# Performance work log

Measured on AMD Instinct MI355X. Metric: run time of the kernel, lower is better.

## Reference

```python
import jax, jax.numpy as jnp
import numpy as np

N, F = 16384, 32
H1, H2, D1, D2 = 64, 64, 32, 1


def setup_inputs() -> dict:
    key = jax.random.key(0)
    ks = jax.random.split(key, 10)
    x = jax.random.normal(ks[0], (N, F), dtype=jnp.float32)
    # pre-normalized adjacency (GCNConv expects D^-1/2 A D^-1/2); mimic with uniform/N
    a = jax.random.uniform(ks[1], (N, N), dtype=jnp.float32) / N
    # glorot-ish scaled params
    W1 = jax.random.normal(ks[2], (F, H1), dtype=jnp.float32) * (1.0 / np.sqrt(F))
    b1 = jnp.zeros((H1,), dtype=jnp.float32)
    W2 = jax.random.normal(ks[3], (H1, H2), dtype=jnp.float32) * (1.0 / np.sqrt(H1))
    b2 = jnp.zeros((H2,), dtype=jnp.float32)
    Wd1 = jax.random.normal(ks[4], (H2, D1), dtype=jnp.float32) * (1.0 / np.sqrt(H2))
    bd1 = jnp.zeros((D1,), dtype=jnp.float32)
    Wd2 = jax.random.normal(ks[5], (D1, D2), dtype=jnp.float32) * (1.0 / np.sqrt(D1))
    bd2 = jnp.zeros((D2,), dtype=jnp.float32)
    return {"x": x, "a": a, "W1": W1, "b1": b1, "W2": W2, "b2": b2,
            "Wd1": Wd1, "bd1": bd1, "Wd2": Wd2, "bd2": bd2}


def reference(x, a, W1, b1, W2, b2, Wd1, bd1, Wd2, bd2):
    # GCNConv: relu(a @ (x @ W) + b)   (a is pre-normalized)
    g1 = jax.nn.relu(a @ (x @ W1) + b1)   # [N, 64]
    g2 = jax.nn.relu(a @ (g1 @ W2) + b2)  # [N, 64]
    d3 = jax.nn.relu(g2 @ Wd1 + bd1)      # [N, 32]
    return d3 @ Wd2 + bd2                 # [N, 1]
```

## Files before the change

kernel.cpp:

```cpp
#include <hip/hip_runtime.h>
#include <hip/hip_bf16.h>


typedef __bf16 bf16x8 __attribute__((ext_vector_type(8)));
typedef float  f32x16 __attribute__((ext_vector_type(16)));
typedef float  f32x4v __attribute__((ext_vector_type(4)));
typedef int    i32x4  __attribute__((ext_vector_type(4)));

#define NNODE 16384
#define KDIM  16384
#define HCOL  64

__device__ inline i32x4 pack8(f32x4v a, f32x4v b){
  bf16x8 t;
  t[0]=(__bf16)a[0]; t[1]=(__bf16)a[1]; t[2]=(__bf16)a[2]; t[3]=(__bf16)a[3];
  t[4]=(__bf16)b[0]; t[5]=(__bf16)b[1]; t[6]=(__bf16)b[2]; t[7]=(__bf16)b[3];
  return __builtin_bit_cast(i32x4, t);
}

__global__ __launch_bounds__(128) void gcn_layer_kernel(
    const float* __restrict__ A,
    const __bf16* __restrict__ Ht,
    const float* __restrict__ bias,
    float* __restrict__ G)
{
  __shared__ i32x4 sA[2*2*256];
  __shared__ i32x4 sH[2*2*512];

  const int tid  = threadIdx.x;
  const int lane = tid & 63;
  const int kw   = tid >> 6;
  const int row0 = blockIdx.x * 32;

  const int rA0  = lane >> 3;
  const int ccA  = lane & 7;
  const int swzA = ccA ^ rA0;
  const int r    = lane & 31;
  const int hsub = lane >> 5;
  const int xs   = lane & 7;

  const size_t k0base = (size_t)kw * 8192;

  f32x4v ra[8]; i32x4 rh[8];

  const float* pA0 = A + (size_t)(row0 + rA0) * KDIM + k0base + (size_t)ccA*8;
  const i32x4* pH0 = (const i32x4*)Ht + (size_t)rA0 * (KDIM/8) + k0base/8 + ccA;

  auto stage_load = [&](int t){
    const float* pA = pA0 + (size_t)t*64;
    #pragma unroll
    for (int pi=0; pi<4; ++pi){
      const float* p = pA + (size_t)pi*8*KDIM;
      ra[2*pi]   = __builtin_nontemporal_load((const f32x4v*)p);
      ra[2*pi+1] = __builtin_nontemporal_load((const f32x4v*)(p+4));
    }
    const i32x4* pH = pH0 + (size_t)t*8;
    #pragma unroll
    for (int pi=0; pi<8; ++pi)
      rh[pi] = pH[(size_t)pi*8*(KDIM/8)];
  };

  auto stage_write = [&](int buf){
    i32x4* dA = &sA[(kw*2+buf)*256];
    #pragma unroll
    for (int pi=0; pi<4; ++pi)
      dA[(rA0 + pi*8)*8 + swzA] = pack8(ra[2*pi], ra[2*pi+1]);
    i32x4* dH = &sH[(kw*2+buf)*512];
    #pragma unroll
    for (int pi=0; pi<8; ++pi)
      dH[(rA0 + pi*8)*8 + swzA] = rh[pi];
  };

  f32x16 acc0 = {}; f32x16 acc1 = {};

  auto compute = [&](int buf){
    const i32x4* bA = &sA[(kw*2+buf)*256];
    const i32x4* bH = &sH[(kw*2+buf)*512];
    #pragma unroll
    for (int kk=0; kk<4; ++kk){
      int c = (kk*2 + hsub) ^ xs;
      bf16x8 a  = __builtin_bit_cast(bf16x8, bA[r*8 + c]);
      bf16x8 b0 = __builtin_bit_cast(bf16x8, bH[r*8 + c]);
      bf16x8 b1 = __builtin_bit_cast(bf16x8, bH[(r+32)*8 + c]);
      acc0 = __builtin_amdgcn_mfma_f32_32x32x16_bf16(a, b0, acc0, 0,0,0);
      acc1 = __builtin_amdgcn_mfma_f32_32x32x16_bf16(a, b1, acc1, 0,0,0);
    }
  };

  stage_load(0);
  stage_write(0);
  __syncthreads();
  for (int t=0; t<127; ++t){
    stage_load(t+1);
    compute(t&1);
    __syncthreads();
    stage_write((t+1)&1);
    __syncthreads();
  }
  compute(1);
  __syncthreads();

  float* red = (float*)sA;
  if (kw == 1){
    #pragma unroll
    for (int j=0; j<16; ++j){
      int rr = (j&3) + 8*(j>>2) + 4*hsub;
      red[rr*64 + r]      = acc0[j];
      red[rr*64 + 32 + r] = acc1[j];
    }
  }
  __syncthreads();
  if (kw == 0){
    #pragma unroll
    for (int j=0; j<16; ++j){
      int rr = (j&3) + 8*(j>>2) + 4*hsub;
      float v0 = acc0[j] + red[rr*64 + r]      + bias[r];
      float v1 = acc1[j] + red[rr*64 + 32 + r] + bias[32 + r];
      G[(size_t)(row0 + rr)*HCOL + r]      = fmaxf(v0, 0.f);
      G[(size_t)(row0 + rr)*HCOL + 32 + r] = fmaxf(v1, 0.f);
    }
  }
}

template<int F>
__global__ __launch_bounds__(128) void proj_T_kernel(
    const float* __restrict__ in,
    const float* __restrict__ W,
    __bf16* __restrict__ out)
{
  constexpr int FP = F + 4;
  __shared__ float sWt[64*FP];
  __shared__ short sOut[64*136];

  int tid = threadIdx.x;
  for (int e = tid; e < 64*F; e += 128){
    int h = e / F, j = e - h*F;
    sWt[h*FP + j] = W[j*64 + h];
  }
  __syncthreads();

  const size_t n = (size_t)blockIdx.x*128 + tid;
  float rowv[F];
  #pragma unroll
  for (int j=0; j<F; j+=4){
    f32x4v v = *(const f32x4v*)(in + n*F + j);
    rowv[j]=v[0]; rowv[j+1]=v[1]; rowv[j+2]=v[2]; rowv[j+3]=v[3];
  }
  #pragma unroll
  for (int h=0; h<64; ++h){
    float s = 0.f;
    #pragma unroll
    for (int j=0; j<F; j+=4){
      f32x4v w = *(const f32x4v*)&sWt[h*FP + j];
      s += rowv[j]*w[0] + rowv[j+1]*w[1] + rowv[j+2]*w[2] + rowv[j+3]*w[3];
    }
    sOut[h*136 + tid] = __builtin_bit_cast(short, (__bf16)s);
  }
  __syncthreads();

  const size_t n0 = (size_t)blockIdx.x*128;
  #pragma unroll
  for (int pi=0; pi<8; ++pi){
    int p = pi*128 + tid;
    int h = p >> 4, cc = p & 15;
    i32x4 v = *(const i32x4*)&sOut[h*136 + cc*8];
    *(i32x4*)(out + (size_t)h*NNODE + n0 + cc*8) = v;
  }
}

__global__ __launch_bounds__(256) void tail_kernel(
    const float* __restrict__ g2,
    const float* __restrict__ Wd1,
    const float* __restrict__ bd1,
    const float* __restrict__ Wd2,
    const float* __restrict__ bd2,
    float* __restrict__ outp)
{
  __shared__ float sW[64*32];
  __shared__ float sb1[32], sw2[32];
  int tid = threadIdx.x;
  for (int e=tid; e<2048; e+=256) sW[e] = Wd1[e];
  if (tid < 32){ sb1[tid] = bd1[tid]; sw2[tid] = Wd2[tid]; }
  __syncthreads();

  size_t n = (size_t)blockIdx.x*256 + tid;
  float rv[64];
  #pragma unroll
  for (int j=0;j<64;j+=4){
    f32x4v v = *(const f32x4v*)(g2 + n*64 + j);
    rv[j]=v[0]; rv[j+1]=v[1]; rv[j+2]=v[2]; rv[j+3]=v[3];
  }
  float o = 0.f;
  #pragma unroll
  for (int c=0;c<32;++c){
    float s = sb1[c];
    #pragma unroll
    for (int j=0;j<64;++j) s += rv[j]*sW[j*32 + c];
    o += fmaxf(s, 0.f) * sw2[c];
  }
  outp[n] = o + bd2[0];
}

extern "C" void kernel_launch(void* const* d_in, const int* in_sizes, int n_in,
                              void* d_out, int out_size, void* d_ws, size_t ws_size,
                              hipStream_t stream)
{
  const float* x   = (const float*)d_in[0];
  const float* a   = (const float*)d_in[1];
  const float* W1  = (const float*)d_in[2];
  const float* b1  = (const float*)d_in[3];
  const float* W2  = (const float*)d_in[4];
  const float* b2  = (const float*)d_in[5];
  const float* Wd1 = (const float*)d_in[6];
  const float* bd1 = (const float*)d_in[7];
  const float* Wd2 = (const float*)d_in[8];
  const float* bd2 = (const float*)d_in[9];
  float* outp = (float*)d_out;

  char* ws = (char*)d_ws;
  __bf16* Ht1 = (__bf16*)(ws);
  __bf16* Ht2 = (__bf16*)(ws + (2u<<20));
  float*  g1  = (float*)(ws + (4u<<20));
  float*  g2  = (float*)(ws + (8u<<20));

  proj_T_kernel<32><<<128, 128, 0, stream>>>(x,  W1, Ht1);
  gcn_layer_kernel <<<512, 128, 0, stream>>>(a, Ht1, b1, g1);
  proj_T_kernel<64><<<128, 128, 0, stream>>>(g1, W2, Ht2);
  gcn_layer_kernel <<<512, 128, 0, stream>>>(a, Ht2, b2, g2);
  tail_kernel      <<<64, 256, 0, stream>>>(g2, Wd1, bd1, Wd2, bd2, outp);
}
```

Measured before the change: 505.9 us.

## Deepen register prefetch to two stages and halve barriers per k-step

Adds a second register buffer so global loads of A and Ht are issued two k-stages ahead of the MFMA compute. Shared-memory writes for the next buffer are interleaved with compute on the other buffer, which drops from two to one __syncthreads per stage. The aim is to hide more HBM latency in this bandwidth-bound aggregation and cut barrier stalls. In exchange it uses more VGPRs and issues a few redundant clamped loads at the tail.

```diff
diff --git a/kernel.cpp b/kernel.cpp
--- a/kernel.cpp
+++ b/kernel.cpp
@@ -41,26 +41,26 @@
 
   const size_t k0base = (size_t)kw * 8192;
 
-  f32x4v ra[8]; i32x4 rh[8];
+  f32x4v ra0[8], ra1[8]; i32x4 rh0[8], rh1[8];
 
   const float* pA0 = A + (size_t)(row0 + rA0) * KDIM + k0base + (size_t)ccA*8;
   const i32x4* pH0 = (const i32x4*)Ht + (size_t)rA0 * (KDIM/8) + k0base/8 + ccA;
 
-  auto stage_load = [&](int t){
-    const float* pA = pA0 + (size_t)t*64;
+  auto stage_load = [&](int idx, f32x4v (&ra)[8], i32x4 (&rh)[8]){
+    const float* pA = pA0 + (size_t)idx*64;
     #pragma unroll
     for (int pi=0; pi<4; ++pi){
       const float* p = pA + (size_t)pi*8*KDIM;
       ra[2*pi]   = __builtin_nontemporal_load((const f32x4v*)p);
       ra[2*pi+1] = __builtin_nontemporal_load((const f32x4v*)(p+4));
     }
-    const i32x4* pH = pH0 + (size_t)t*8;
+    const i32x4* pH = pH0 + (size_t)idx*8;
     #pragma unroll
     for (int pi=0; pi<8; ++pi)
       rh[pi] = pH[(size_t)pi*8*(KDIM/8)];
   };
 
-  auto stage_write = [&](int buf){
+  auto stage_write = [&](int buf, f32x4v (&ra)[8], i32x4 (&rh)[8]){
     i32x4* dA = &sA[(kw*2+buf)*256];
     #pragma unroll
     for (int pi=0; pi<4; ++pi)
@@ -87,18 +87,25 @@
     }
   };
 
-  stage_load(0);
-  stage_write(0);
-  __syncthreads();
-  for (int t=0; t<127; ++t){
-    stage_load(t+1);
-    compute(t&1);
+  stage_load(0, ra0, rh0);
+  stage_load(1, ra1, rh1);
+  stage_write(0, ra0, rh0);
+  stage_load(2, ra0, rh0);
+  __syncthreads();
+
+  #pragma unroll 1
+  for (int t=0; t<128; t+=2){
+    int i3 = t+3; if (i3 > 127) i3 = 127;
+    int i4 = t+4; if (i4 > 127) i4 = 127;
+    stage_write(1, ra1, rh1);
+    stage_load(i3, ra1, rh1);
+    compute(0);
     __syncthreads();
-    stage_write((t+1)&1);
+    stage_write(0, ra0, rh0);
+    stage_load(i4, ra0, rh0);
+    compute(1);
     __syncthreads();
   }
-  compute(1);
-  __syncthreads();
 
   float* red = (float*)sA;
   if (kw == 1){
```

Measured after the change: 536.2 us. +6.0%, slower.

## Load MFMA operands directly from global memory and split K across four waves

Applied to the files above, without the earlier changes.

Removes the LDS staging buffers and per-step barriers in the GCN aggregation kernel. Each lane now loads its MFMA fragments straight from global memory into registers, with double buffering. The block grows to 256 threads so four waves split K, with a three-way LDS reduction at the end. This trades barrier and LDS traffic for less coalesced, fragmented global reads of the large adjacency matrix.

```diff
diff --git a/kernel.cpp b/kernel.cpp
--- a/kernel.cpp
+++ b/kernel.cpp
@@ -11,102 +11,82 @@
 #define KDIM  16384
 #define HCOL  64
 
-__device__ inline i32x4 pack8(f32x4v a, f32x4v b){
+__device__ inline bf16x8 pack8(f32x4v a, f32x4v b){
   bf16x8 t;
   t[0]=(__bf16)a[0]; t[1]=(__bf16)a[1]; t[2]=(__bf16)a[2]; t[3]=(__bf16)a[3];
   t[4]=(__bf16)b[0]; t[5]=(__bf16)b[1]; t[6]=(__bf16)b[2]; t[7]=(__bf16)b[3];
-  return __builtin_bit_cast(i32x4, t);
-}
-
-__global__ __launch_bounds__(128) void gcn_layer_kernel(
+  return t;
+}
+
+__global__ __launch_bounds__(256, 2) void gcn_layer_kernel(
     const float* __restrict__ A,
     const __bf16* __restrict__ Ht,
     const float* __restrict__ bias,
     float* __restrict__ G)
 {
-  __shared__ i32x4 sA[2*2*256];
-  __shared__ i32x4 sH[2*2*512];
+  __shared__ float red[3*32*64];
 
   const int tid  = threadIdx.x;
   const int lane = tid & 63;
   const int kw   = tid >> 6;
   const int row0 = blockIdx.x * 32;
-
-  const int rA0  = lane >> 3;
-  const int ccA  = lane & 7;
-  const int swzA = ccA ^ rA0;
   const int r    = lane & 31;
   const int hsub = lane >> 5;
-  const int xs   = lane & 7;
-
-  const size_t k0base = (size_t)kw * 8192;
-
-  f32x4v ra[8]; i32x4 rh[8];
-
-  const float* pA0 = A + (size_t)(row0 + rA0) * KDIM + k0base + (size_t)ccA*8;
-  const i32x4* pH0 = (const i32x4*)Ht + (size_t)rA0 * (KDIM/8) + k0base/8 + ccA;
-
-  auto stage_load = [&](int t){
-    const float* pA = pA0 + (size_t)t*64;
-    #pragma unroll
-    for (int pi=0; pi<4; ++pi){
-      const float* p = pA + (size_t)pi*8*KDIM;
-      ra[2*pi]   = __builtin_nontemporal_load((const f32x4v*)p);
-      ra[2*pi+1] = __builtin_nontemporal_load((const f32x4v*)(p+4));
-    }
-    const i32x4* pH = pH0 + (size_t)t*8;
-    #pragma unroll
-    for (int pi=0; pi<8; ++pi)
-      rh[pi] = pH[(size_t)pi*8*(KDIM/8)];
+
+  const size_t k0 = (size_t)kw * 4096;
+  const float*  pa  = A  + (size_t)(row0 + r) * KDIM + k0 + (size_t)hsub*8;
+  const __bf16* pb0 = Ht + (size_t)r        * KDIM + k0 + (size_t)hsub*8;
+  const __bf16* pb1 = Ht + (size_t)(r + 32) * KDIM + k0 + (size_t)hsub*8;
+
+  f32x16 acc0 = {}; f32x16 acc1 = {};
+
+  f32x4v a0[8], a1[8];
+  i32x4  b00[4], b01[4], b10[4], b11[4];
+
+  auto LOAD = [&](f32x4v (&a)[8], i32x4 (&b0)[4], i32x4 (&b1)[4], int t){
+    const float* p = pa + (size_t)t*64;
+    #pragma unroll
+    for (int kk=0; kk<4; ++kk){
+      a[2*kk]   = __builtin_nontemporal_load((const f32x4v*)(p + kk*16));
+      a[2*kk+1] = __builtin_nontemporal_load((const f32x4v*)(p + kk*16 + 4));
+    }
+    const __bf16* q0 = pb0 + (size_t)t*64;
+    const __bf16* q1 = pb1 + (size_t)t*64;
+    #pragma unroll
+    for (int kk=0; kk<4; ++kk){
+      b0[kk] = *(const i32x4*)(q0 + kk*16);
+      b1[kk] = *(const i32x4*)(q1 + kk*16);
+    }
   };
 
-  auto stage_write = [&](int buf){
-    i32x4* dA = &sA[(kw*2+buf)*256];
-    #pragma unroll
-    for (int pi=0; pi<4; ++pi)
-      dA[(rA0 + pi*8)*8 + swzA] = pack8(ra[2*pi], ra[2*pi+1]);
-    i32x4* dH = &sH[(kw*2+buf)*512];
-    #pragma unroll
-    for (int pi=0; pi<8; ++pi)
-      dH[(rA0 + pi*8)*8 + swzA] = rh[pi];
+  auto COMP = [&](f32x4v (&a)[8], i32x4 (&b0)[4], i32x4 (&b1)[4]){
+    #pragma unroll
+    for (int kk=0; kk<4; ++kk){
+      bf16x8 af = pack8(a[2*kk], a[2*kk+1]);
+      acc0 = __builtin_amdgcn_mfma_f32_32x32x16_bf16(af, __builtin_bit_cast(bf16x8, b0[kk]), acc0, 0,0,0);
+      acc1 = __builtin_amdgcn_mfma_f32_32x32x16_bf16(af, __builtin_bit_cast(bf16x8, b1[kk]), acc1, 0,0,0);
+    }
   };
 
-  f32x16 acc0 = {}; f32x16 acc1 = {};
-
-  auto compute = [&](int buf){
-    const i32x4* bA = &sA[(kw*2+buf)*256];
-    const i32x4* bH = &sH[(kw*2+buf)*512];
-    #pragma unroll
-    for (int kk=0; kk<4; ++kk){
-      int c = (kk*2 + hsub) ^ xs;
-      bf16x8 a  = __builtin_bit_cast(bf16x8, bA[r*8 + c]);
-      bf16x8 b0 = __builtin_bit_cast(bf16x8, bH[r*8 + c]);
-      bf16x8 b1 = __builtin_bit_cast(bf16x8, bH[(r+32)*8 + c]);
-      acc0 = __builtin_amdgcn_mfma_f32_32x32x16_bf16(a, b0, acc0, 0,0,0);
-      acc1 = __builtin_amdgcn_mfma_f32_32x32x16_bf16(a, b1, acc1, 0,0,0);
-    }
-  };
-
-  stage_load(0);
-  stage_write(0);
-  __syncthreads();
-  for (int t=0; t<127; ++t){
-    stage_load(t+1);
-    compute(t&1);
-    __syncthreads();
-    stage_write((t+1)&1);
-    __syncthreads();
-  }
-  compute(1);
-  __syncthreads();
-
-  float* red = (float*)sA;
-  if (kw == 1){
+  LOAD(a0, b00, b01, 0);
+  LOAD(a1, b10, b11, 1);
+  #pragma unroll 1
+  for (int t=0; t<62; t+=2){
+    COMP(a0, b00, b01);
+    LOAD(a0, b00, b01, t+2);
+    COMP(a1, b10, b11);
+    LOAD(a1, b10, b11, t+3);
+  }
+  COMP(a0, b00, b01);
+  COMP(a1, b10, b11);
+
+  if (kw > 0){
+    float* rd = red + (kw-1)*2048;
     #pragma unroll
     for (int j=0; j<16; ++j){
       int rr = (j&3) + 8*(j>>2) + 4*hsub;
-      red[rr*64 + r]      = acc0[j];
-      red[rr*64 + 32 + r] = acc1[j];
+      rd[rr*64 + r]      = acc0[j];
+      rd[rr*64 + 32 + r] = acc1[j];
     }
   }
   __syncthreads();
@@ -114,8 +94,8 @@
     #pragma unroll
     for (int j=0; j<16; ++j){
       int rr = (j&3) + 8*(j>>2) + 4*hsub;
-      float v0 = acc0[j] + red[rr*64 + r]      + bias[r];
-      float v1 = acc1[j] + red[rr*64 + 32 + r] + bias[32 + r];
+      float v0 = acc0[j] + red[rr*64+r]      + red[2048+rr*64+r]      + red[4096+rr*64+r]      + bias[r];
+      float v1 = acc1[j] + red[rr*64+32+r]   + red[2048+rr*64+32+r]   + red[4096+rr*64+32+r]   + bias[32+r];
       G[(size_t)(row0 + rr)*HCOL + r]      = fmaxf(v0, 0.f);
       G[(size_t)(row0 + rr)*HCOL + 32 + r] = fmaxf(v1, 0.f);
     }
@@ -224,8 +204,8 @@
   float*  g2  = (float*)(ws + (8u<<20));
 
   proj_T_kernel<32><<<128, 128, 0, stream>>>(x,  W1, Ht1);
-  gcn_layer_kernel <<<512, 128, 0, stream>>>(a, Ht1, b1, g1);
+  gcn_layer_kernel <<<512, 256, 0, stream>>>(a, Ht1, b1, g1);
   proj_T_kernel<64><<<128, 128, 0, stream>>>(g1, W2, Ht2);
-  gcn_layer_kernel <<<512, 128, 0, stream>>>(a, Ht2, b2, g2);
+  gcn_layer_kernel <<<512, 256, 0, stream>>>(a, Ht2, b2, g2);
   tail_kernel      <<<64, 256, 0, stream>>>(g2, Wd1, bd1, Wd2, bd2, outp);
 }
```

Measured after the change: 840.6 us. +66.2%, slower.
